# Performance work log

Hardware: AMD Instinct MI355X
Metric: run time of the kernel (lower is better)

## Reference

```python
import jax, jax.numpy as jnp
import numpy as np
import math

N = 65536
B = 128            # graphs, each of 512 nodes
D = 512            # model_dim
DK = 64            # d_k
H = 8              # heads
DV = D // H        # d_v = 64
DFF = 2048
L = 4              # transformer layers
MOVES = 10
PD = 1024          # policy hidden
VD = 1024          # value hidden
EPS = 1e-5


def _xavier(key, shape, fan_in, fan_out):
    lim = math.sqrt(6.0 / (fan_in + fan_out))
    return jax.random.uniform(key, shape, jnp.float32, -lim, lim)


def setup_inputs() -> dict:
    key = jax.random.key(0)
    ks = jax.random.split(key, 24)
    inp = {
        "x6": jax.random.normal(ks[0], (N, 6), jnp.float32),
        "adjacency": jax.random.randint(ks[1], (N, 4), 0, N, jnp.int32),
        "batch_sizes": jnp.full((B,), N // B, jnp.int32),
        # input embedding Linear(6, D)
        "embed_w": _xavier(ks[2], (6, D), 6, D),
        "embed_b": jnp.zeros((D,), jnp.float32),
        # per-layer attention params (stacked over L)
        "wq": _xavier(ks[3], (L, H, D, DK), D, DK),
        "wk": _xavier(ks[4], (L, H, 5, D, DK), 5 * D, DK),
        "wv": _xavier(ks[5], (L, H, 5, D, DV), 5 * D, DV),
        # per-layer FFN
        "ffn_w1": _xavier(ks[6], (L, D, DFF), D, DFF),
        "ffn_b1": jnp.zeros((L, DFF), jnp.float32),
        "ffn_w2": _xavier(ks[7], (L, DFF, D), DFF, D),
        "ffn_b2": jnp.zeros((L, D), jnp.float32),
        # per-layer LayerNorms
        "ln1_g": jnp.ones((L, D), jnp.float32),
        "ln1_b": jnp.zeros((L, D), jnp.float32),
        "ln2_g": jnp.ones((L, D), jnp.float32),
        "ln2_b": jnp.zeros((L, D), jnp.float32),
        # policy head MLP (per-node logits over moves)
        "pol_w1": _xavier(ks[8], (D, PD), D, PD),
        "pol_b1": jnp.zeros((PD,), jnp.float32),
        "pol_w2": _xavier(ks[9], (PD, MOVES), PD, MOVES),
        "pol_b2": jnp.zeros((MOVES,), jnp.float32),
        # value head MLP on mean-pooled graph embedding
        "val_w1": _xavier(ks[10], (D, VD), D, VD),
        "val_b1": jnp.zeros((VD,), jnp.float32),
        "val_w2": _xavier(ks[11], (VD, 1), VD, 1),
        "val_b2": jnp.zeros((1,), jnp.float32),
    }
    return inp


def _layernorm(x, g, b):
    mu = jnp.mean(x, axis=-1, keepdims=True)
    var = jnp.mean(jnp.square(x - mu), axis=-1, keepdims=True)
    return (x - mu) * jax.lax.rsqrt(var + EPS) * g + b


def _forward(x6, adjacency, batch_sizes, embed_w, embed_b, wq, wk, wv,
             ffn_w1, ffn_b1, ffn_w2, ffn_b2, ln1_g, ln1_b, ln2_g, ln2_b,
             pol_w1, pol_b1, pol_w2, pol_b2, val_w1, val_b1, val_w2, val_b2):
    x = x6 @ embed_w + embed_b                      # (N, D)
    scale = 1.0 / math.sqrt(DK)
    for i in range(L):
        real = x[adjacency]                          # (N, 4, D) gather neighbors
        xn = jnp.concatenate([x[:, None, :], real], axis=1)  # (N, 5, D)
        Q = jnp.einsum('nd,hdk->hnk', x, wq[i])
        K = jnp.einsum('nrd,hrdk->hnrk', xn, wk[i])
        V = jnp.einsum('nrd,hrdv->hnrv', xn, wv[i])
        A = jnp.einsum('hnk,hnrk->hnr', Q, K) * scale
        # NOTE: original code does F.softmax(A, dim=1) -> over the node axis
        A = jax.nn.softmax(A, axis=1)
        Z = jnp.einsum('hnr,hnrv->hnv', A, V)
        Z = Z.transpose(1, 0, 2).reshape(x.shape[0], -1)  # (N, H*DV) = (N, D)
        x = _layernorm(x + Z, ln1_g[i], ln1_b[i])
        f = jax.nn.relu(x @ ffn_w1[i] + ffn_b1[i]) @ ffn_w2[i] + ffn_b2[i]
        x = _layernorm(x + f, ln2_g[i], ln2_b[i])
    # policy head: per-node action logits
    policy = jax.nn.relu(x @ pol_w1 + pol_b1) @ pol_w2 + pol_b2   # (N, MOVES)
    # value head: segment mean pool (mean_pool_index_add) then MLP + tanh
    seg = jnp.repeat(jnp.arange(B), batch_sizes, total_repeat_length=N)
    summed = jax.ops.segment_sum(x, seg, num_segments=B)          # (B, D)
    pooled = summed / jnp.clip(batch_sizes.astype(x.dtype)[:, None], 1e-9)
    value = jnp.tanh(jax.nn.relu(pooled @ val_w1 + val_b1) @ val_w2 + val_b2)[:, 0]
    return policy, value


def reference(x6, adjacency, batch_sizes, embed_w, embed_b, wq, wk, wv,
              ffn_w1, ffn_b1, ffn_w2, ffn_b2, ln1_g, ln1_b, ln2_g, ln2_b,
              pol_w1, pol_b1, pol_w2, pol_b2, val_w1, val_b1, val_w2, val_b2):
    return _forward(x6, adjacency, batch_sizes, embed_w, embed_b, wq, wk, wv,
                    ffn_w1, ffn_b1, ffn_w2, ffn_b2, ln1_g, ln1_b, ln2_g, ln2_b,
                    pol_w1, pol_b1, pol_w2, pol_b2, val_w1, val_b1, val_w2, val_b2)
```

## Files before the change

kernel.cpp:

```cpp
#include <hip/hip_runtime.h>

typedef unsigned short u16;
typedef __bf16 bf16x8 __attribute__((ext_vector_type(8)));
typedef float f32x4 __attribute__((ext_vector_type(4)));
typedef short s8v __attribute__((ext_vector_type(8)));
typedef short s4v __attribute__((ext_vector_type(4)));

#define NND 65536
#define CHF 32768

#define VM2 asm volatile("s_waitcnt vmcnt(2)" ::: "memory")
#define VM0 asm volatile("s_waitcnt vmcnt(0)" ::: "memory")
#define BAR __builtin_amdgcn_s_barrier()
#define SCB __builtin_amdgcn_sched_barrier(0)

__device__ __forceinline__ float bs2f(short s) {
    union { unsigned u; float f; } x;
    x.u = ((unsigned)(u16)s) << 16;
    return x.f;
}
__device__ __forceinline__ u16 f2bu(float f) {
    union { float f; unsigned u; } x;
    x.f = f;
    unsigned r = x.u + 0x7FFFu + ((x.u >> 16) & 1u);
    return (u16)(r >> 16);
}
__device__ __forceinline__ void g2l16(const void* g, void* l) {
    __builtin_amdgcn_global_load_lds((const __attribute__((address_space(1))) void*)g,
                                     (__attribute__((address_space(3))) void*)l, 16, 0, 0);
}
__device__ __forceinline__ void xcd_decode(int lognbn, int& bm, int& bn) {
    int flat = blockIdx.x;
    int cpx = gridDim.x >> 3;
    int virt = (flat & 7) * cpx + (flat >> 3);
    bm = virt >> lognbn;
    bn = virt & ((1 << lognbn) - 1);
}

__global__ void k_conv_qkv(const float* __restrict__ wq, const float* __restrict__ wk,
                           const float* __restrict__ wv, u16* __restrict__ wqT,
                           u16* __restrict__ wkT, u16* __restrict__ wvT, int l)
{
    int bz = blockIdx.y;
    const float* in; u16* out;
    if (bz < 40) {
        int h = bz / 5, r = bz % 5;
        in  = wk + (size_t)((l * 8 + h) * 5 + r) * 32768;
        out = wkT + (size_t)r * 262144 + h * 64 * 512;
    } else if (bz < 80) {
        int t = bz - 40; int h = t / 5, r = t % 5;
        in  = wv + (size_t)((l * 8 + h) * 5 + r) * 32768;
        out = wvT + (size_t)r * 262144 + h * 64 * 512;
    } else {
        int h = bz - 80;
        in  = wq + (size_t)(l * 8 + h) * 32768;
        out = wqT + h * 64 * 512;
    }
    int d0 = blockIdx.x * 32;
    __shared__ float s[32][65];
    int tid = threadIdx.x;
    int di = tid >> 3, k8 = (tid & 7) * 8;
    const float* ip = in + (long)(d0 + di) * 64 + k8;
    #pragma unroll
    for (int i = 0; i < 8; ++i) s[di][k8 + i] = ip[i];
    __syncthreads();
    int kk = tid >> 2, d8 = (tid & 3) * 8;
    s8v o;
    #pragma unroll
    for (int i = 0; i < 8; ++i) o[i] = (short)f2bu(s[d8 + i][kk]);
    *(s8v*)(out + (long)kk * 512 + d0 + d8) = o;
}

__global__ void k_convT(const float* __restrict__ in, u16* __restrict__ out, int R, int C)
{
    int tiles_c = C >> 5;
    int tr = blockIdx.x / tiles_c, tc = blockIdx.x % tiles_c;
    int r0 = tr * 32, c0 = tc * 32;
    __shared__ float s[32][33];
    int tid = threadIdx.x;
    int ri = tid >> 3, c4 = (tid & 7) * 4;
    const float4 v = *(const float4*)(in + (long)(r0 + ri) * C + c0 + c4);
    s[ri][c4] = v.x; s[ri][c4 + 1] = v.y; s[ri][c4 + 2] = v.z; s[ri][c4 + 3] = v.w;
    __syncthreads();
    int ci = tid >> 3, r4 = (tid & 7) * 4;
    s4v o;
    #pragma unroll
    for (int i = 0; i < 4; ++i) o[i] = (short)f2bu(s[r4 + i][ci]);
    *(s4v*)(out + (long)(c0 + ci) * R + r0 + r4) = o;
}

__global__ void k_conv_w2f(const float* __restrict__ w2, u16* __restrict__ w2f)
{
    int tid = threadIdx.x;
    for (int t = tid; t < 2048; t += 512) {
        int s = t >> 6, l = t & 63;
        int m = l & 15;
        int kbase = s * 32 + ((l >> 4) << 3);
        s8v o;
        #pragma unroll
        for (int j = 0; j < 8; ++j) {
            float v = (m < 10) ? w2[(long)(kbase + j) * 10 + m] : 0.f;
            o[j] = (short)f2bu(v);
        }
        *(s8v*)(w2f + (long)s * 512 + l * 8) = o;
    }
}

__global__ void k_embed(const float* __restrict__ x6, const float* __restrict__ ew,
                        const float* __restrict__ eb, u16* __restrict__ xbf)
{
    int n = blockIdx.x, j = threadIdx.x;
    const float* r = x6 + (long)n * 6;
    float a = eb[j] + r[0] * ew[j] + r[1] * ew[512 + j] + r[2] * ew[1024 + j]
            + r[3] * ew[1536 + j] + r[4] * ew[2048 + j] + r[5] * ew[2560 + j];
    xbf[(long)n * 512 + j] = f2bu(a);
}

template<bool BIAS, bool RELU, bool ADDX>
__global__ __launch_bounds__(512, 4)
void k_gemm(const u16* __restrict__ A, const u16* __restrict__ BT,
            u16* __restrict__ C, const float* __restrict__ bias,
            const u16* __restrict__ resid, int K, int Ncols, int lognbn)
{
    __shared__ u16 sA[3][4096];
    __shared__ u16 sB[3][4096];
    const int tid = threadIdx.x;
    const int wave = tid >> 6, lane = tid & 63;
    int bm, bn;
    xcd_decode(lognbn, bm, bn);

    const int arow = tid >> 2;
    const int acol8 = ((tid & 3) ^ ((tid >> 3) & 3)) * 8;
    const u16* pa = A + ((long)bm * 128 + arow) * K + acol8;
    const u16* pb = BT + ((long)bn * 128 + arow) * K + acol8;

    char* sAc = (char*)sA;
    char* sBc = (char*)sB;
    const int dst = tid * 16;

    f32x4 acc[2][4] = {};

    const int wm = wave >> 1, wn = wave & 1;
    const int fr = lane & 15;
    const int g4 = lane >> 4;
    const int kbs = (g4 ^ ((fr >> 1) & 3)) * 16;
    const char* ra = sAc + (wm * 32 + fr) * 64 + kbs;
    const char* rb = sBc + (wn * 64 + fr) * 64 + kbs;

    auto STAGE = [&](int buf) {
        g2l16(pa, sAc + buf * 8192 + dst);
        g2l16(pb, sBc + buf * 8192 + dst);
        pa += 32; pb += 32;
    };

    const int NT = K >> 5;
    STAGE(0); STAGE(1);
    VM2; BAR; SCB;

    int cur = 0, nx2 = 2;
    for (int t = 0; t < NT; ++t) {
        if (t + 2 < NT) STAGE(nx2);
        bf16x8 af[2], bfr[4];
        const char* rac = ra + cur * 8192;
        const char* rbc = rb + cur * 8192;
        #pragma unroll
        for (int mi = 0; mi < 2; ++mi) af[mi] = *(const bf16x8*)(rac + mi * 1024);
        #pragma unroll
        for (int ni = 0; ni < 4; ++ni) bfr[ni] = *(const bf16x8*)(rbc + ni * 1024);
        __builtin_amdgcn_s_setprio(1);
        #pragma unroll
        for (int mi = 0; mi < 2; ++mi)
            #pragma unroll
            for (int ni = 0; ni < 4; ++ni)
                acc[mi][ni] = __builtin_amdgcn_mfma_f32_16x16x32_bf16(af[mi], bfr[ni], acc[mi][ni], 0, 0, 0);
        __builtin_amdgcn_s_setprio(0);
        if (t + 2 < NT)      { VM2; }
        else if (t + 1 < NT) { VM0; }
        BAR; SCB;
        cur = (cur == 2) ? 0 : cur + 1;
        nx2 = (nx2 == 2) ? 0 : nx2 + 1;
    }

    const int crow0 = bm * 128 + wm * 32 + g4 * 4;
    const int ccol0 = bn * 128 + wn * 64 + fr;
    #pragma unroll
    for (int mi = 0; mi < 2; ++mi) {
        #pragma unroll
        for (int ni = 0; ni < 4; ++ni) {
            int col = ccol0 + ni * 16;
            float bv = BIAS ? bias[col] : 0.f;
            #pragma unroll
            for (int j = 0; j < 4; ++j) {
                int row = crow0 + mi * 16 + j;
                float v = acc[mi][ni][j] + bv;
                if (ADDX) v += bs2f(resid[(long)row * Ncols + col]);
                if (RELU) v = fmaxf(v, 0.f);
                C[(long)row * Ncols + col] = f2bu(v);
            }
        }
    }
}

__global__ __launch_bounds__(512, 4)
void k_attnKS(const u16* __restrict__ xbf, const u16* __restrict__ wqT,
              const u16* __restrict__ wkT, const int* __restrict__ adj,
              float* __restrict__ S)
{
    __shared__ u16 sA[3][4096];
    __shared__ u16 sB[3][4096];
    const int tid = threadIdx.x;
    const int wave = tid >> 6, lane = tid & 63;
    int bm, bn;
    xcd_decode(2, bm, bn);
    const int arow = tid >> 2;
    const int acol8 = ((tid & 3) ^ ((tid >> 3) & 3)) * 8;

    char* sAc = (char*)sA;
    char* sBc = (char*)sB;
    const int dst = tid * 16;

    const int wm = wave >> 1, wn = wave & 1;
    const int fr = lane & 15;
    const int g4 = lane >> 4;
    const int kbs = (g4 ^ ((fr >> 1) & 3)) * 16;
    const char* ra = sAc + (wm * 32 + fr) * 64 + kbs;
    const char* rb = sBc + (wn * 64 + fr) * 64 + kbs;

    const int h = bn * 2 + wn;
    const int rowbase = bm * 128 + wm * 32;

    unsigned qp[2][4][2];

    for (int ph = 0; ph < 6; ++ph) {
        long r0 = (long)bm * 128 + arow;
        if (ph >= 2) r0 = adj[r0 * 4 + (ph - 2)];
        const u16* pa = xbf + r0 * 512 + acol8;
        const u16* bw = (ph == 0) ? wqT : wkT + (size_t)(ph - 1) * 262144;
        const u16* pb = bw + ((long)bn * 128 + arow) * 512 + acol8;

        auto STAGE = [&](int buf) {
            g2l16(pa, sAc + buf * 8192 + dst);
            g2l16(pb, sBc + buf * 8192 + dst);
            pa += 32; pb += 32;
        };

        STAGE(0); STAGE(1);
        VM2; BAR; SCB;

        f32x4 acc[2][4] = {};
        int cur = 0, nx2 = 2;
        for (int t = 0; t < 16; ++t) {
            if (t + 2 < 16) STAGE(nx2);
            bf16x8 af[2], bfr[4];
            const char* rac = ra + cur * 8192;
            const char* rbc = rb + cur * 8192;
            #pragma unroll
            for (int mi = 0; mi < 2; ++mi) af[mi] = *(const bf16x8*)(rac + mi * 1024);
            #pragma unroll
            for (int ni = 0; ni < 4; ++ni) bfr[ni] = *(const bf16x8*)(rbc + ni * 1024);
            __builtin_amdgcn_s_setprio(1);
            #pragma unroll
            for (int mi = 0; mi < 2; ++mi)
                #pragma unroll
                for (int ni = 0; ni < 4; ++ni)
                    acc[mi][ni] = __builtin_amdgcn_mfma_f32_16x16x32_bf16(af[mi], bfr[ni], acc[mi][ni], 0, 0, 0);
            __builtin_amdgcn_s_setprio(0);
            if (t + 2 < 16)      { VM2; }
            else if (t + 1 < 16) { VM0; }
            BAR; SCB;
            cur = (cur == 2) ? 0 : cur + 1;
            nx2 = (nx2 == 2) ? 0 : nx2 + 1;
        }

        if (ph == 0) {
            #pragma unroll
            for (int mi = 0; mi < 2; ++mi)
                #pragma unroll
                for (int ni = 0; ni < 4; ++ni)
                    #pragma unroll
                    for (int jj = 0; jj < 2; ++jj)
                        qp[mi][ni][jj] = (unsigned)f2bu(acc[mi][ni][2 * jj])
                                       | ((unsigned)f2bu(acc[mi][ni][2 * jj + 1]) << 16);
        } else {
            int sc = h * 5 + (ph - 1);
            #pragma unroll
            for (int mi = 0; mi < 2; ++mi) {
                float pj[4];
                #pragma unroll
                for (int j = 0; j < 4; ++j) {
                    float s = 0.f;
                    #pragma unroll
                    for (int ni = 0; ni < 4; ++ni) {
                        unsigned w = qp[mi][ni][j >> 1];
                        u16 qh = (j & 1) ? (u16)(w >> 16) : (u16)(w & 0xffff);
                        s += acc[mi][ni][j] * bs2f((short)qh);
                    }
                    #pragma unroll
                    for (int m = 1; m < 16; m <<= 1) s += __shfl_xor(s, m);
                    pj[j] = s * 0.125f;
                }
                if (fr == 0) {
                    float4 o; o.x = pj[0]; o.y = pj[1]; o.z = pj[2]; o.w = pj[3];
                    *(float4*)&S[(size_t)sc * NND + rowbase + mi * 16 + g4 * 4] = o;
                }
            }
        }
    }
}

__global__ void k_colstats(const float* __restrict__ S, float* __restrict__ stats)
{
    int col = blockIdx.x;
    int tid = threadIdx.x;
    const float* Sc = S + (size_t)col * NND;
    float m = -1e30f, s = 0.f;
    for (int n = tid; n < NND; n += 256) {
        float v = Sc[n];
        if (v > m) { s = s * __expf(m - v) + 1.f; m = v; }
        else s += __expf(v - m);
    }
    __shared__ float smx[256], ssm[256];
    smx[tid] = m; ssm[tid] = s;
    __syncthreads();
    for (int off = 128; off; off >>= 1) {
        if (tid < off) {
            float m2 = smx[tid + off], s2 = ssm[tid + off];
            float M = fmaxf(smx[tid], m2);
            ssm[tid] = ssm[tid] * __expf(smx[tid] - M) + s2 * __expf(m2 - M);
            smx[tid] = M;
        }
        __syncthreads();
    }
    if (tid == 0) stats[col] = smx[0] + __logf(ssm[0]);
}

__global__ __launch_bounds__(512, 4)
void k_attnVZ(const u16* __restrict__ xbf, const u16* __restrict__ wvT,
              const int* __restrict__ adj, const float* __restrict__ S,
              const float* __restrict__ stats, u16* __restrict__ t0)
{
    __shared__ u16 sA[3][4096];
    __shared__ u16 sB[3][4096];
    const int tid = threadIdx.x;
    const int wave = tid >> 6, lane = tid & 63;
    int bm, bn;
    xcd_decode(2, bm, bn);
    const int arow = tid >> 2;
    const int acol8 = ((tid & 3) ^ ((tid >> 3) & 3)) * 8;

    char* sAc = (char*)sA;
    char* sBc = (char*)sB;
    const int dst = tid * 16;

    const int wm = wave >> 1, wn = wave & 1;
    const int fr = lane & 15;
    const int g4 = lane >> 4;
    const int kbs = (g4 ^ ((fr >> 1) & 3)) * 16;
    const char* ra = sAc + (wm * 32 + fr) * 64 + kbs;
    const char* rb = sBc + (wn * 64 + fr) * 64 + kbs;

    const int h = bn * 2 + wn;
    const int rowbase = bm * 128 + wm * 32;

    f32x4 acc[2][4] = {};

    for (int ph = 0; ph < 5; ++ph) {
        long r0 = (long)bm * 128 + arow;
        if (ph >= 1) r0 = adj[r0 * 4 + (ph - 1)];
        const u16* pa = xbf + r0 * 512 + acol8;
        const u16* pb = wvT + (size_t)ph * 262144 + ((long)bn * 128 + arow) * 512 + acol8;

        auto STAGE = [&](int buf) {
            g2l16(pa, sAc + buf * 8192 + dst);
            g2l16(pb, sBc + buf * 8192 + dst);
            pa += 32; pb += 32;
        };

        STAGE(0); STAGE(1);
        VM2; BAR; SCB;

        int cur = 0, nx2 = 2;
        for (int t = 0; t < 16; ++t) {
            if (t + 2 < 16) STAGE(nx2);
            bf16x8 af[2], bfr[4];
            const char* rac = ra + cur * 8192;
            const char* rbc = rb + cur * 8192;
            #pragma unroll
            for (int mi = 0; mi < 2; ++mi) af[mi] = *(const bf16x8*)(rac + mi * 1024);
            #pragma unroll
            for (int ni = 0; ni < 4; ++ni) bfr[ni] = *(const bf16x8*)(rbc + ni * 1024);
            __builtin_amdgcn_s_setprio(1);
            #pragma unroll
            for (int mi = 0; mi < 2; ++mi)
                #pragma unroll
                for (int ni = 0; ni < 4; ++ni)
                    acc[mi][ni] = __builtin_amdgcn_mfma_f32_16x16x32_bf16(af[mi], bfr[ni], acc[mi][ni], 0, 0, 0);
            __builtin_amdgcn_s_setprio(0);
            if (t + 2 < 16)      { VM2; }
            else if (t + 1 < 16) { VM0; }
            BAR; SCB;
            cur = (cur == 2) ? 0 : cur + 1;
            nx2 = (nx2 == 2) ? 0 : nx2 + 1;
        }

        int sc = h * 5 + ph;
        if (ph < 4) {
            float Lc = stats[sc], Ln = stats[sc + 1];
            #pragma unroll
            for (int mi = 0; mi < 2; ++mi) {
                int rb4 = rowbase + mi * 16 + g4 * 4;
                float4 c4 = *(const float4*)&S[(size_t)sc * NND + rb4];
                float4 n4 = *(const float4*)&S[(size_t)(sc + 1) * NND + rb4];
                float rt[4];
                rt[0] = __expf((c4.x - Lc) - (n4.x - Ln));
                rt[1] = __expf((c4.y - Lc) - (n4.y - Ln));
                rt[2] = __expf((c4.z - Lc) - (n4.z - Ln));
                rt[3] = __expf((c4.w - Lc) - (n4.w - Ln));
                #pragma unroll
                for (int ni = 0; ni < 4; ++ni)
                    #pragma unroll
                    for (int j = 0; j < 4; ++j)
                        acc[mi][ni][j] *= rt[j];
            }
        } else {
            float Lc = stats[sc];
            #pragma unroll
            for (int mi = 0; mi < 2; ++mi) {
                int rb4 = rowbase + mi * 16 + g4 * 4;
                float4 c4 = *(const float4*)&S[(size_t)sc * NND + rb4];
                float a[4];
                a[0] = __expf(c4.x - Lc);
                a[1] = __expf(c4.y - Lc);
                a[2] = __expf(c4.z - Lc);
                a[3] = __expf(c4.w - Lc);
                #pragma unroll
                for (int ni = 0; ni < 4; ++ni) {
                    int col = bn * 128 + wn * 64 + ni * 16 + fr;
                    #pragma unroll
                    for (int j = 0; j < 4; ++j) {
                        long row = rb4 + j;
                        float v = acc[mi][ni][j] * a[j] + bs2f(xbf[row * 512 + col]);
                        t0[row * 512 + col] = f2bu(v);
                    }
                }
            }
        }
    }
}

__global__ void k_ln(const u16* __restrict__ t, u16* __restrict__ x,
                     const float* __restrict__ g, const float* __restrict__ b)
{
    int n = blockIdx.x, tid = threadIdx.x;
    long base = (long)n * 512 + tid * 4;
    s4v tv = *(const s4v*)(t + base);
    float v0 = bs2f(tv[0]), v1 = bs2f(tv[1]), v2 = bs2f(tv[2]), v3 = bs2f(tv[3]);
    float s1 = v0 + v1 + v2 + v3;
    float s2 = v0 * v0 + v1 * v1 + v2 * v2 + v3 * v3;
    #pragma unroll
    for (int off = 32; off; off >>= 1) {
        s1 += __shfl_down(s1, off);
        s2 += __shfl_down(s2, off);
    }
    __shared__ float a1[2], a2[2];
    int w = tid >> 6, lane = tid & 63;
    if (lane == 0) { a1[w] = s1; a2[w] = s2; }
    __syncthreads();
    float S1 = a1[0] + a1[1], S2 = a2[0] + a2[1];
    float mu = S1 * (1.f / 512.f);
    float var = S2 * (1.f / 512.f) - mu * mu;
    float rs = rsqrtf(var + 1e-5f);
    int c = tid * 4;
    s4v ob;
    ob[0] = (short)f2bu((v0 - mu) * rs * g[c] + b[c]);
    ob[1] = (short)f2bu((v1 - mu) * rs * g[c + 1] + b[c + 1]);
    ob[2] = (short)f2bu((v2 - mu) * rs * g[c + 2] + b[c + 2]);
    ob[3] = (short)f2bu((v3 - mu) * rs * g[c + 3] + b[c + 3]);
    *(s4v*)(x + base) = ob;
}

__global__ __launch_bounds__(512)
void k_pol2m(const u16* __restrict__ p1, const u16* __restrict__ w2f,
             const float* __restrict__ b2, float* __restrict__ out)
{
    const int wave = threadIdx.x >> 6, lane = threadIdx.x & 63;
    const long n0 = ((long)blockIdx.x * 8 + wave) * 16;
    const int row = lane & 15;
    const int ko = (lane >> 4) * 8;
    const u16* pa = p1 + (n0 + row) * 1024 + ko;
    f32x4 acc = {};
    #pragma unroll 4
    for (int s = 0; s < 32; ++s) {
        bf16x8 a = *(const bf16x8*)(pa + s * 32);
        bf16x8 b = *(const bf16x8*)(w2f + s * 512 + lane * 8);
        acc = __builtin_amdgcn_mfma_f32_16x16x32_bf16(a, b, acc, 0, 0, 0);
    }
    const int col = lane & 15;
    if (col < 10) {
        float bv = b2[col];
        #pragma unroll
        for (int j = 0; j < 4; ++j)
            out[(n0 + (lane >> 4) * 4 + j) * 10 + col] = acc[j] + bv;
    }
}

__global__ void k_offsets(const int* __restrict__ bs, int* __restrict__ offs)
{
    if (threadIdx.x == 0) {
        int acc = 0;
        for (int i = 0; i < 128; ++i) { offs[i] = acc; acc += bs[i]; }
        offs[128] = acc;
    }
}

__global__ void k_pool(const u16* __restrict__ x, const int* __restrict__ offs,
                       const int* __restrict__ bs, float* __restrict__ pooled)
{
    int g = blockIdx.x, tid = threadIdx.x;
    int c = tid * 4;
    int r0 = offs[g], r1 = offs[g + 1];
    float a0 = 0.f, a1 = 0.f, a2 = 0.f, a3 = 0.f;
    for (int rr = r0; rr < r1; ++rr) {
        s4v v = *(const s4v*)(x + (long)rr * 512 + c);
        a0 += bs2f(v[0]); a1 += bs2f(v[1]); a2 += bs2f(v[2]); a3 += bs2f(v[3]);
    }
    float d = fmaxf((float)bs[g], 1e-9f);
    pooled[g * 512 + c] = a0 / d;
    pooled[g * 512 + c + 1] = a1 / d;
    pooled[g * 512 + c + 2] = a2 / d;
    pooled[g * 512 + c + 3] = a3 / d;
}

__global__ void k_val1(const float* __restrict__ pooled, const float* __restrict__ w1,
                       const float* __restrict__ b1, float* __restrict__ v1)
{
    int g = blockIdx.x;
    int j = blockIdx.y * 256 + threadIdx.x;
    __shared__ float sp[512];
    for (int i = threadIdx.x; i < 512; i += 256) sp[i] = pooled[g * 512 + i];
    __syncthreads();
    float a = b1[j];
    for (int d = 0; d < 512; ++d) a += sp[d] * w1[(long)d * 1024 + j];
    v1[g * 1024 + j] = fmaxf(a, 0.f);
}

__global__ void k_val2(const float* __restrict__ v1, const float* __restrict__ w2,
                       const float* __restrict__ b2, float* __restrict__ out)
{
    int g = blockIdx.x, lane = threadIdx.x;
    float a = 0.f;
    for (int k = lane; k < 1024; k += 64) a += v1[g * 1024 + k] * w2[k];
    #pragma unroll
    for (int off = 32; off; off >>= 1) a += __shfl_down(a, off);
    if (lane == 0) out[(long)NND * 10 + g] = tanhf(a + b2[0]);
}

extern "C" void kernel_launch(void* const* d_in, const int* in_sizes, int n_in,
                              void* d_out, int out_size, void* d_ws, size_t ws_size,
                              hipStream_t stream)
{
    (void)in_sizes; (void)n_in; (void)out_size; (void)ws_size;
    const float* x6        = (const float*)d_in[0];
    const int*   adjacency = (const int*)d_in[1];
    const int*   batch_sz  = (const int*)d_in[2];
    const float* embed_w   = (const float*)d_in[3];
    const float* embed_b   = (const float*)d_in[4];
    const float* wq        = (const float*)d_in[5];
    const float* wk        = (const float*)d_in[6];
    const float* wv        = (const float*)d_in[7];
    const float* ffn_w1    = (const float*)d_in[8];
    const float* ffn_b1    = (const float*)d_in[9];
    const float* ffn_w2    = (const float*)d_in[10];
    const float* ffn_b2    = (const float*)d_in[11];
    const float* ln1_g     = (const float*)d_in[12];
    const float* ln1_b     = (const float*)d_in[13];
    const float* ln2_g     = (const float*)d_in[14];
    const float* ln2_b     = (const float*)d_in[15];
    const float* pol_w1    = (const float*)d_in[16];
    const float* pol_b1    = (const float*)d_in[17];
    const float* pol_w2    = (const float*)d_in[18];
    const float* pol_b2    = (const float*)d_in[19];
    const float* val_w1    = (const float*)d_in[20];
    const float* val_b1    = (const float*)d_in[21];
    const float* val_w2    = (const float*)d_in[22];
    const float* val_b2    = (const float*)d_in[23];
    float* out = (float*)d_out;

    char* ws = (char*)d_ws;
    size_t off = 0;
    auto alloc = [&](size_t bytes) {
        char* p = ws + off;
        off = (off + bytes + 255) & ~(size_t)255;
        return p;
    };
    u16*   xbf  = (u16*)  alloc((size_t)NND * 512 * 2);
    u16*   t0   = (u16*)  alloc((size_t)NND * 512 * 2);
    char*  arena=         alloc((size_t)NND * 512 * 2);
    float* S    = (float*)alloc((size_t)40 * NND * 4);
    float* stats= (float*)alloc(4096);
    float* pooled=(float*)alloc(128 * 512 * 4);
    float* v1   = (float*)alloc(128 * 1024 * 4);
    int*   offs = (int*)  alloc(1024);
    u16*   wqTl = (u16*)  alloc((size_t)262144 * 2);
    u16*   wkTl = (u16*)  alloc((size_t)5 * 262144 * 2);
    u16*   wvTl = (u16*)  alloc((size_t)5 * 262144 * 2);
    u16*   w1Tl = (u16*)  alloc((size_t)2048 * 512 * 2);
    u16*   w2Tl = (u16*)  alloc((size_t)512 * 2048 * 2);
    u16*   pw1T = (u16*)  alloc((size_t)1024 * 512 * 2);
    u16*   w2f  = (u16*)  alloc((size_t)16384 * 2);

    u16* hb  = t0;
    u16* p1c = (u16*)arena;

    k_convT<<<512, 256, 0, stream>>>(pol_w1, pw1T, 512, 1024);
    k_conv_w2f<<<1, 512, 0, stream>>>(pol_w2, w2f);
    k_offsets<<<1, 128, 0, stream>>>(batch_sz, offs);
    k_embed<<<NND, 512, 0, stream>>>(x6, embed_w, embed_b, xbf);

    for (int l = 0; l < 4; ++l) {
        k_conv_qkv<<<dim3(16, 88), 256, 0, stream>>>(wq, wk, wv, wqTl, wkTl, wvTl, l);
        k_convT<<<1024, 256, 0, stream>>>(ffn_w1 + (size_t)l * 512 * 2048, w1Tl, 512, 2048);
        k_convT<<<1024, 256, 0, stream>>>(ffn_w2 + (size_t)l * 2048 * 512, w2Tl, 2048, 512);

        k_attnKS<<<2048, 512, 0, stream>>>(xbf, wqTl, wkTl, adjacency, S);
        k_colstats<<<40, 256, 0, stream>>>(S, stats);
        k_attnVZ<<<2048, 512, 0, stream>>>(xbf, wvTl, adjacency, S, stats, t0);
        k_ln<<<NND, 128, 0, stream>>>(t0, xbf, ln1_g + l * 512, ln1_b + l * 512);
        for (int c = 0; c < NND / CHF; ++c) {
            size_t row0 = (size_t)c * CHF;
            k_gemm<true,true,false><<<4096, 512, 0, stream>>>(
                xbf + row0 * 512, w1Tl, hb, ffn_b1 + l * 2048, nullptr, 512, 2048, 4);
            k_gemm<true,false,true><<<1024, 512, 0, stream>>>(
                hb, w2Tl, xbf + row0 * 512, ffn_b2 + l * 512, xbf + row0 * 512, 2048, 512, 2);
        }
        k_ln<<<NND, 128, 0, stream>>>(xbf, xbf, ln2_g + l * 512, ln2_b + l * 512);
    }

    for (int c = 0; c < NND / CHF; ++c) {
        size_t row0 = (size_t)c * CHF;
        k_gemm<true,true,false><<<2048, 512, 0, stream>>>(
            xbf + row0 * 512, pw1T, p1c, pol_b1, nullptr, 512, 1024, 3);
        k_pol2m<<<CHF / 128, 512, 0, stream>>>(p1c, w2f, pol_b2, out + row0 * 10);
    }
    k_pool<<<128, 128, 0, stream>>>(xbf, offs, batch_sz, pooled);
    k_val1<<<dim3(128, 4), 256, 0, stream>>>(pooled, val_w1, val_b1, v1);
    k_val2<<<128, 64, 0, stream>>>(v1, val_w2, val_b2, out);
}
```

Before: 4.315 ms.

## Load GEMM A fragments directly from global into registers, bypassing LDS

The GEMM kernel no longer stages the A tile through shared memory. Each wave loads its own A MFMA fragments straight from global memory into registers with double-buffered even/odd register sets, while B still goes through the triple-buffered LDS pipeline. The loop is unrolled by two and the vmcnt waits are adjusted to match. This halves LDS traffic and footprint, which may allow higher occupancy, but A is no longer shared between the two waves that use the same rows, so redundant global/L2 loads rise and the uncoalesced per-lane fragment loads may expose more latency. The unrolled loop also looks like it assumes an even tile count, and the waitcnt accounting is delicate.

```diff
diff --git a/kernel.cpp b/kernel.cpp
--- a/kernel.cpp
+++ b/kernel.cpp
@@ -9,6 +9,7 @@
 #define NND 65536
 #define CHF 32768
 
+#define VM3 asm volatile("s_waitcnt vmcnt(3)" ::: "memory")
 #define VM2 asm volatile("s_waitcnt vmcnt(2)" ::: "memory")
 #define VM0 asm volatile("s_waitcnt vmcnt(0)" ::: "memory")
 #define BAR __builtin_amdgcn_s_barrier()
@@ -28,6 +29,11 @@
 __device__ __forceinline__ void g2l16(const void* g, void* l) {
     __builtin_amdgcn_global_load_lds((const __attribute__((address_space(1))) void*)g,
                                      (__attribute__((address_space(3))) void*)l, 16, 0, 0);
+}
+__device__ __forceinline__ bf16x8 gld16(const u16* p) {
+    bf16x8 r;
+    asm volatile("global_load_dwordx4 %0, %1, off" : "=v"(r) : "v"(p));
+    return r;
 }
 __device__ __forceinline__ void xcd_decode(int lognbn, int& bm, int& bn) {
     int flat = blockIdx.x;
@@ -122,19 +128,16 @@
             u16* __restrict__ C, const float* __restrict__ bias,
             const u16* __restrict__ resid, int K, int Ncols, int lognbn)
 {
-    __shared__ u16 sA[3][4096];
     __shared__ u16 sB[3][4096];
     const int tid = threadIdx.x;
     const int wave = tid >> 6, lane = tid & 63;
     int bm, bn;
     xcd_decode(lognbn, bm, bn);
 
-    const int arow = tid >> 2;
-    const int acol8 = ((tid & 3) ^ ((tid >> 3) & 3)) * 8;
-    const u16* pa = A + ((long)bm * 128 + arow) * K + acol8;
-    const u16* pb = BT + ((long)bn * 128 + arow) * K + acol8;
-
-    char* sAc = (char*)sA;
+    const int brow = tid >> 2;
+    const int bcol8 = ((tid & 3) ^ ((tid >> 3) & 3)) * 8;
+    const u16* pb = BT + ((long)bn * 128 + brow) * K + bcol8;
+
     char* sBc = (char*)sB;
     const int dst = tid * 16;
 
@@ -144,41 +147,74 @@
     const int fr = lane & 15;
     const int g4 = lane >> 4;
     const int kbs = (g4 ^ ((fr >> 1) & 3)) * 16;
-    const char* ra = sAc + (wm * 32 + fr) * 64 + kbs;
     const char* rb = sBc + (wn * 64 + fr) * 64 + kbs;
 
+    const u16* paf0 = A + ((long)bm * 128 + wm * 32 + fr) * K + g4 * 8;
+    const u16* paf1 = paf0 + (long)16 * K;
+
     auto STAGE = [&](int buf) {
-        g2l16(pa, sAc + buf * 8192 + dst);
         g2l16(pb, sBc + buf * 8192 + dst);
-        pa += 32; pb += 32;
+        pb += 32;
     };
 
     const int NT = K >> 5;
     STAGE(0); STAGE(1);
+    SCB;
+    bf16x8 aE0 = gld16(paf0), aE1 = gld16(paf1);
+    bf16x8 aO0 = gld16(paf0 + 32), aO1 = gld16(paf1 + 32);
+    SCB;
     VM2; BAR; SCB;
 
     int cur = 0, nx2 = 2;
-    for (int t = 0; t < NT; ++t) {
-        if (t + 2 < NT) STAGE(nx2);
-        bf16x8 af[2], bfr[4];
-        const char* rac = ra + cur * 8192;
-        const char* rbc = rb + cur * 8192;
-        #pragma unroll
-        for (int mi = 0; mi < 2; ++mi) af[mi] = *(const bf16x8*)(rac + mi * 1024);
-        #pragma unroll
-        for (int ni = 0; ni < 4; ++ni) bfr[ni] = *(const bf16x8*)(rbc + ni * 1024);
-        __builtin_amdgcn_s_setprio(1);
-        #pragma unroll
-        for (int mi = 0; mi < 2; ++mi)
+    for (int t = 0; t < NT; t += 2) {
+        if (t + 2 < NT) { STAGE(nx2); nx2 = (nx2 == 2) ? 0 : nx2 + 1; }
+        SCB;
+        {
+            bf16x8 bfr[4];
+            const char* rbc = rb + cur * 8192;
+            #pragma unroll
+            for (int ni = 0; ni < 4; ++ni) bfr[ni] = *(const bf16x8*)(rbc + ni * 1024);
+            __builtin_amdgcn_s_setprio(1);
             #pragma unroll
             for (int ni = 0; ni < 4; ++ni)
-                acc[mi][ni] = __builtin_amdgcn_mfma_f32_16x16x32_bf16(af[mi], bfr[ni], acc[mi][ni], 0, 0, 0);
-        __builtin_amdgcn_s_setprio(0);
-        if (t + 2 < NT)      { VM2; }
-        else if (t + 1 < NT) { VM0; }
+                acc[0][ni] = __builtin_amdgcn_mfma_f32_16x16x32_bf16(aE0, bfr[ni], acc[0][ni], 0, 0, 0);
+            #pragma unroll
+            for (int ni = 0; ni < 4; ++ni)
+                acc[1][ni] = __builtin_amdgcn_mfma_f32_16x16x32_bf16(aE1, bfr[ni], acc[1][ni], 0, 0, 0);
+            __builtin_amdgcn_s_setprio(0);
+        }
+        if (t + 2 < NT) {
+            aE0 = gld16(paf0 + (t + 2) * 32);
+            aE1 = gld16(paf1 + (t + 2) * 32);
+            SCB; VM3;
+        } else if (t + 1 < NT) {
+            VM0;
+        }
         BAR; SCB;
         cur = (cur == 2) ? 0 : cur + 1;
-        nx2 = (nx2 == 2) ? 0 : nx2 + 1;
+        if (t + 3 < NT) { STAGE(nx2); nx2 = (nx2 == 2) ? 0 : nx2 + 1; }
+        SCB;
+        {
+            bf16x8 bfr[4];
+            const char* rbc = rb + cur * 8192;
+            #pragma unroll
+            for (int ni = 0; ni < 4; ++ni) bfr[ni] = *(const bf16x8*)(rbc + ni * 1024);
+            __builtin_amdgcn_s_setprio(1);
+            #pragma unroll
+            for (int ni = 0; ni < 4; ++ni)
+                acc[0][ni] = __builtin_amdgcn_mfma_f32_16x16x32_bf16(aO0, bfr[ni], acc[0][ni], 0, 0, 0);
+            #pragma unroll
+            for (int ni = 0; ni < 4; ++ni)
+                acc[1][ni] = __builtin_amdgcn_mfma_f32_16x16x32_bf16(aO1, bfr[ni], acc[1][ni], 0, 0, 0);
+            __builtin_amdgcn_s_setprio(0);
+        }
+        if (t + 3 < NT) {
+            aO0 = gld16(paf0 + (t + 3) * 32);
+            aO1 = gld16(paf1 + (t + 3) * 32);
+            SCB; VM3;
+        }
+        BAR; SCB;
+        cur = (cur == 2) ? 0 : cur + 1;
     }
 
     const int crow0 = bm * 128 + wm * 32 + g4 * 4;
```

Result: slower. 5.042 ms (+16.8%).
